# Performance work log

Measured on AMD Instinct MI355X. Metric: run time of the kernel, lower is better.

Reference implementation:

```python
import jax, jax.numpy as jnp
import numpy as np

B, V, D = 128, 1024, 512

def setup_inputs() -> dict:
    key = jax.random.key(0)
    ks = jax.random.split(key, 6)
    return {
        "features": jax.random.normal(ks[0], (B, D), dtype=jnp.float32),
        "phoneme_counts": jax.random.uniform(ks[1], (V,), minval=0.01, maxval=1.0, dtype=jnp.float32),
        "total_count": jnp.asarray(float(V), dtype=jnp.float32),
        "meg_prototypes": jax.random.normal(ks[2], (V, D), dtype=jnp.float32),
        "zipf_s": jnp.asarray(1.0, dtype=jnp.float32),
        "temperature": jnp.asarray(1.0, dtype=jnp.float32),
        "W1": jax.random.normal(ks[3], (D, 2 * D), dtype=jnp.float32) * 0.02,
        "b1": jnp.zeros((D,), dtype=jnp.float32),
        "W2": jax.random.normal(ks[4], (1, D), dtype=jnp.float32) * 0.02,
        "b2": jnp.zeros((1,), dtype=jnp.float32),
    }

def _l2norm(x, axis=-1, eps=1e-12):
    n = jnp.sqrt(jnp.sum(x * x, axis=axis, keepdims=True))
    return x / jnp.maximum(n, eps)

def reference(features, phoneme_counts, total_count, meg_prototypes,
              zipf_s, temperature, W1, b1, W2, b2):
    vocab = phoneme_counts.shape[0]
    d = features.shape[1]
    # Zipf weights: rank phonemes by frequency (descending), weight = rank^{-s}
    freqs = phoneme_counts / jnp.maximum(total_count, 1.0)
    order = jnp.argsort(-freqs)  # indices sorted by descending frequency
    ranks = jnp.zeros_like(freqs).at[order].set(
        jnp.arange(1, vocab + 1, dtype=freqs.dtype))
    zw = jnp.power(jnp.maximum(ranks, 1.0), -zipf_s)
    zipf_priors = zw / jnp.maximum(zw.sum(), 1e-8)  # [V]
    # Cosine similarity / temperature
    sim = _l2norm(features) @ _l2norm(meg_prototypes).T  # [B, V]
    sim = sim / jnp.maximum(temperature, 1e-4)
    # MLP attention: split Linear(2D,D) into feature and prototype halves,
    # avoiding the materialized [B,V,2D] concat.
    Wf, Wp = W1[:, :d], W1[:, d:]  # each [D, D]
    feat_part = features @ Wf.T          # [B, D]
    proto_part = meg_prototypes @ Wp.T   # [V, D]
    h = jax.nn.relu(feat_part[:, None, :] + proto_part[None, :, :] + b1)  # [B, V, D]
    attn = jax.nn.sigmoid(jnp.einsum('bvd,d->bv', h, W2[0]) + b2[0])      # [B, V]
    weights = zipf_priors[None, :] * (1.0 + sim) * attn
    return jax.nn.softmax(weights, axis=-1)
```

## Files before the change

### kernel.cpp

```cpp
#include <hip/hip_runtime.h>
#include <hip/hip_bf16.h>


typedef __attribute__((ext_vector_type(8))) short bhalf8;
typedef __attribute__((ext_vector_type(4))) float f32x4;

static __device__ __forceinline__ unsigned short f2bf(float x) {
    union { __hip_bfloat16 h; unsigned short u; } cv;
    cv.h = __float2bfloat16(x);
    return cv.u;
}

static __device__ __forceinline__ int4 pack_bf16_8(float4 x, float4 y) {
    union { ushort u[8]; int4 v; } r;
    r.u[0] = f2bf(x.x); r.u[1] = f2bf(x.y); r.u[2] = f2bf(x.z); r.u[3] = f2bf(x.w);
    r.u[4] = f2bf(y.x); r.u[5] = f2bf(y.y); r.u[6] = f2bf(y.z); r.u[7] = f2bf(y.w);
    return r.v;
}

__global__ __launch_bounds__(256) void gemm_prep_kernel(
    const float* __restrict__ feat, const float* __restrict__ counts,
    const float* __restrict__ proto, const float* __restrict__ zs,
    const float* __restrict__ W1, const float* __restrict__ b1,
    float* __restrict__ fpT, unsigned short* __restrict__ ppbT,
    float* __restrict__ dotraw,
    float* __restrict__ zw, float* __restrict__ invf, float* __restrict__ invp)
{
    int bx = blockIdx.x, tid = threadIdx.x;

    if (bx >= 176) {
        if (bx < 192) {
            __shared__ float cn[1024];
            ((float4*)cn)[tid] = ((const float4*)counts)[tid];
            __syncthreads();
            int il = tid >> 2, q = tid & 3;
            int i = (bx - 176) * 64 + il;
            float ci = cn[i];
            int cnt = 0;
            int j0 = q * 256;
            for (int j = j0; j < j0 + 256; ++j) {
                float cj = cn[j];
                cnt += (cj > ci) ? 1 : 0;
                cnt += (cj == ci && j < i) ? 1 : 0;
            }
            cnt += __shfl_xor(cnt, 1);
            cnt += __shfl_xor(cnt, 2);
            if (q == 0) zw[i] = powf((float)(cnt + 1), -zs[0]);
        } else {
            int nb = bx - 192;
            int w = tid >> 6, lane = tid & 63;
            int row = nb * 4 + w;
            const float* src = (row < 128) ? (feat + (size_t)row * 512)
                                           : (proto + (size_t)(row - 128) * 512);
            const float4* rp = (const float4*)src;
            float4 a = rp[lane * 2], b = rp[lane * 2 + 1];
            float ss = a.x*a.x + a.y*a.y + a.z*a.z + a.w*a.w
                     + b.x*b.x + b.y*b.y + b.z*b.z + b.w*b.w;
            for (int o = 32; o; o >>= 1) ss += __shfl_xor(ss, o);
            if (lane == 0) {
                float inv = 1.0f / fmaxf(sqrtf(ss), 1e-12f);
                if (row < 128) invf[row] = inv; else invp[row - 128] = inv;
            }
        }
        return;
    }

    const float* A; const float* Bm;
    int lda, ldb, tm, tn, mode;
    if (bx < 16) {
        A = feat; lda = 512; Bm = W1; ldb = 1024; mode = 0;
        tm = bx >> 3; tn = bx & 7;
    } else if (bx < 144) {
        int t = bx - 16;
        A = W1 + 512; lda = 1024; Bm = proto; ldb = 512; mode = 1;
        tm = t >> 4; tn = t & 15;
    } else {
        int t = bx - 144;
        A = feat; lda = 512; Bm = proto; ldb = 512; mode = 2;
        tm = t >> 4; tn = t & 15;
    }

    __shared__ unsigned short As[2][64 * 72];
    __shared__ unsigned short Bs[2][64 * 72];

    int r = tid >> 2, kq = (tid & 3) * 16;
    int wave = tid >> 6, lane = tid & 63;
    int fr = lane & 15, quad = lane >> 4;

    const float* Ag = A + (size_t)(tm * 64 + r) * lda + kq;
    const float* Bg = Bm + (size_t)(tn * 64 + r) * ldb + kq;

    float4 a0 = *(const float4*)(Ag),      a1 = *(const float4*)(Ag + 4);
    float4 a2 = *(const float4*)(Ag + 8),  a3 = *(const float4*)(Ag + 12);
    float4 g0 = *(const float4*)(Bg),      g1 = *(const float4*)(Bg + 4);
    float4 g2 = *(const float4*)(Bg + 8),  g3 = *(const float4*)(Bg + 12);

    f32x4 acc0 = {0.f, 0.f, 0.f, 0.f};
    f32x4 acc1 = acc0, acc2 = acc0, acc3 = acc0;

    for (int kc = 0; kc < 512; kc += 64) {
        int p = (kc >> 6) & 1;
        *(int4*)&As[p][r * 72 + kq]     = pack_bf16_8(a0, a1);
        *(int4*)&As[p][r * 72 + kq + 8] = pack_bf16_8(a2, a3);
        *(int4*)&Bs[p][r * 72 + kq]     = pack_bf16_8(g0, g1);
        *(int4*)&Bs[p][r * 72 + kq + 8] = pack_bf16_8(g2, g3);
        __syncthreads();
        if (kc + 64 < 512) {
            const float* An = Ag + kc + 64;
            const float* Bn = Bg + kc + 64;
            a0 = *(const float4*)(An);     a1 = *(const float4*)(An + 4);
            a2 = *(const float4*)(An + 8); a3 = *(const float4*)(An + 12);
            g0 = *(const float4*)(Bn);     g1 = *(const float4*)(Bn + 4);
            g2 = *(const float4*)(Bn + 8); g3 = *(const float4*)(Bn + 12);
        }
        #pragma unroll
        for (int s = 0; s < 2; ++s) {
            int ko = s * 32 + quad * 8;
            bhalf8 af  = *(const bhalf8*)&As[p][(wave * 16 + fr) * 72 + ko];
            bhalf8 bf0 = *(const bhalf8*)&Bs[p][(fr) * 72 + ko];
            bhalf8 bf1 = *(const bhalf8*)&Bs[p][(16 + fr) * 72 + ko];
            bhalf8 bf2 = *(const bhalf8*)&Bs[p][(32 + fr) * 72 + ko];
            bhalf8 bf3 = *(const bhalf8*)&Bs[p][(48 + fr) * 72 + ko];
            acc0 = __builtin_amdgcn_mfma_f32_16x16x32_bf16(af, bf0, acc0, 0, 0, 0);
            acc1 = __builtin_amdgcn_mfma_f32_16x16x32_bf16(af, bf1, acc1, 0, 0, 0);
            acc2 = __builtin_amdgcn_mfma_f32_16x16x32_bf16(af, bf2, acc2, 0, 0, 0);
            acc3 = __builtin_amdgcn_mfma_f32_16x16x32_bf16(af, bf3, acc3, 0, 0, 0);
        }
    }

    int m0 = tm * 64 + wave * 16 + quad * 4;
    int n0 = tn * 64 + fr;
    f32x4 accs[4] = {acc0, acc1, acc2, acc3};
    if (mode == 0) {
        for (int j = 0; j < 4; ++j)
            for (int rr = 0; rr < 4; ++rr)
                fpT[(size_t)(n0 + j * 16) * 128 + m0 + rr] = accs[j][rr];
    } else if (mode == 1) {
        float bv4[4];
        for (int rr = 0; rr < 4; ++rr) bv4[rr] = b1[m0 + rr];
        for (int j = 0; j < 4; ++j)
            for (int rr = 0; rr < 4; ++rr)
                ppbT[(size_t)(m0 + rr) * 1024 + n0 + j * 16] = f2bf(accs[j][rr] + bv4[rr]);
    } else {
        for (int j = 0; j < 4; ++j)
            for (int rr = 0; rr < 4; ++rr)
                dotraw[(size_t)(m0 + rr) * 1024 + n0 + j * 16] = accs[j][rr];
    }
}

__global__ __launch_bounds__(256) void hs_kernel(
    const float* __restrict__ fpT, const unsigned short* __restrict__ ppbT,
    const float* __restrict__ W2, float* __restrict__ hsp)
{
    int bx = blockIdx.x, tid = threadIdx.x;
    int bg = bx & 31, vh = (bx >> 5) & 1, ks = bx >> 6;
    int b0 = bg * 4, v = vh * 512 + tid * 2, k0 = ks * 32;

    float acc[4][2] = {};
    #pragma unroll 8
    for (int kk = 0; kk < 32; ++kk) {
        int k = k0 + kk;
        unsigned int u = *(const unsigned int*)(ppbT + (size_t)k * 1024 + v);
        float px = __uint_as_float(u << 16);
        float py = __uint_as_float(u & 0xffff0000u);
        float w2k = W2[k];
        float4 fa = *(const float4*)(fpT + (size_t)k * 128 + b0);
        float f[4] = {fa.x, fa.y, fa.z, fa.w};
        #pragma unroll
        for (int i = 0; i < 4; ++i) {
            acc[i][0] += fmaxf(f[i] + px, 0.f) * w2k;
            acc[i][1] += fmaxf(f[i] + py, 0.f) * w2k;
        }
    }
    float* o = hsp + ((size_t)ks * 128 + b0) * 1024 + v;
    #pragma unroll
    for (int i = 0; i < 4; ++i)
        *(float2*)(o + (size_t)i * 1024) = make_float2(acc[i][0], acc[i][1]);
}

__global__ __launch_bounds__(1024) void combine_kernel(
    const float* __restrict__ dotraw, const float* __restrict__ hsp,
    const float* __restrict__ zw,
    const float* __restrict__ invf, const float* __restrict__ invp,
    const float* __restrict__ temp, const float* __restrict__ b2,
    float* __restrict__ out)
{
    int b = blockIdx.x, tid = threadIdx.x;
    int wave = tid >> 6, lane = tid & 63;
    int v = tid;
    __shared__ float red[16];

    float it  = invf[b] / fmaxf(temp[0], 1e-4f);
    float b2v = b2[0];

    float zwv = zw[v];
    float dr  = dotraw[(size_t)b * 1024 + v];
    float ipv = invp[v];

    float h = 0.f;
    #pragma unroll
    for (int s = 0; s < 16; ++s)
        h += hsp[((size_t)s * 128 + b) * 1024 + v];

    float zs4 = zwv;
    for (int o = 32; o; o >>= 1) zs4 += __shfl_xor(zs4, o);
    if (lane == 0) red[wave] = zs4;
    __syncthreads();
    float zsum = 0.f;
    #pragma unroll
    for (int i = 0; i < 16; ++i) zsum += red[i];
    float izw = 1.0f / fmaxf(zsum, 1e-8f);
    __syncthreads();

    float sim = dr * it * ipv;
    float g = h + b2v;
    float w = (zwv * izw) * (1.0f + sim) * (1.0f / (1.0f + expf(-g)));

    float mx = w;
    for (int o = 32; o; o >>= 1) mx = fmaxf(mx, __shfl_xor(mx, o));
    if (lane == 0) red[wave] = mx;
    __syncthreads();
    mx = red[0];
    #pragma unroll
    for (int i = 1; i < 16; ++i) mx = fmaxf(mx, red[i]);
    __syncthreads();

    float e = expf(w - mx);
    float sm = e;
    for (int o = 32; o; o >>= 1) sm += __shfl_xor(sm, o);
    if (lane == 0) red[wave] = sm;
    __syncthreads();
    float tot = 0.f;
    #pragma unroll
    for (int i = 0; i < 16; ++i) tot += red[i];

    out[(size_t)b * 1024 + v] = e / tot;
}

extern "C" void kernel_launch(void* const* d_in, const int* in_sizes, int n_in,
                              void* d_out, int out_size, void* d_ws, size_t ws_size,
                              hipStream_t stream) {
    const float* feat   = (const float*)d_in[0];
    const float* counts = (const float*)d_in[1];
    const float* proto  = (const float*)d_in[3];
    const float* zs     = (const float*)d_in[4];
    const float* temp   = (const float*)d_in[5];
    const float* W1     = (const float*)d_in[6];
    const float* b1     = (const float*)d_in[7];
    const float* W2     = (const float*)d_in[8];
    const float* b2     = (const float*)d_in[9];

    char* ws = (char*)d_ws;
    float* zw     = (float*)(ws + 0);
    float* invf   = (float*)(ws + 4096);
    float* invp   = (float*)(ws + 4608);
    float* fpT    = (float*)(ws + 8704);
    float* dotraw = (float*)(ws + 270848);
    unsigned short* ppbT = (unsigned short*)(ws + 795136);
    float* hsp    = (float*)(ws + 1843712);

    gemm_prep_kernel<<<480, 256, 0, stream>>>(feat, counts, proto, zs, W1, b1,
                                              fpT, ppbT, dotraw, zw, invf, invp);
    hs_kernel<<<1024, 256, 0, stream>>>(fpT, ppbT, W2, hsp);
    combine_kernel<<<128, 1024, 0, stream>>>(dotraw, hsp, zw, invf, invp,
                                             temp, b2, (float*)d_out);
}
```

Before: 100.9 us.

## Fuse hidden-state reduction into combine kernel, drop partial-sum buffer

Moves the relu-MLP dot product into the final softmax kernel, one block per batch row with two k-halves reduced via shared memory. fp is now written row-major so each block reads its contiguous feature row. This removes a launch and the large partial-sum buffer round trip through global memory. In exchange it launches only 128 blocks and loses the 4-row register reuse of prototype loads, lengthening the serial per-thread loop.

```diff
diff --git a/kernel.cpp b/kernel.cpp
--- a/kernel.cpp
+++ b/kernel.cpp
@@ -22,7 +22,7 @@
     const float* __restrict__ feat, const float* __restrict__ counts,
     const float* __restrict__ proto, const float* __restrict__ zs,
     const float* __restrict__ W1, const float* __restrict__ b1,
-    float* __restrict__ fpT, unsigned short* __restrict__ ppbT,
+    float* __restrict__ fp, unsigned short* __restrict__ ppbT,
     float* __restrict__ dotraw,
     float* __restrict__ zw, float* __restrict__ invf, float* __restrict__ invp)
 {
@@ -134,7 +134,7 @@
     if (mode == 0) {
         for (int j = 0; j < 4; ++j)
             for (int rr = 0; rr < 4; ++rr)
-                fpT[(size_t)(n0 + j * 16) * 128 + m0 + rr] = accs[j][rr];
+                fp[(size_t)(m0 + rr) * 512 + n0 + j * 16] = accs[j][rr];
     } else if (mode == 1) {
         float bv4[4];
         for (int rr = 0; rr < 4; ++rr) bv4[rr] = b1[m0 + rr];
@@ -148,59 +148,47 @@
     }
 }
 
-__global__ __launch_bounds__(256) void hs_kernel(
-    const float* __restrict__ fpT, const unsigned short* __restrict__ ppbT,
-    const float* __restrict__ W2, float* __restrict__ hsp)
-{
-    int bx = blockIdx.x, tid = threadIdx.x;
-    int bg = bx & 31, vh = (bx >> 5) & 1, ks = bx >> 6;
-    int b0 = bg * 4, v = vh * 512 + tid * 2, k0 = ks * 32;
-
-    float acc[4][2] = {};
-    #pragma unroll 8
-    for (int kk = 0; kk < 32; ++kk) {
-        int k = k0 + kk;
-        unsigned int u = *(const unsigned int*)(ppbT + (size_t)k * 1024 + v);
-        float px = __uint_as_float(u << 16);
-        float py = __uint_as_float(u & 0xffff0000u);
-        float w2k = W2[k];
-        float4 fa = *(const float4*)(fpT + (size_t)k * 128 + b0);
-        float f[4] = {fa.x, fa.y, fa.z, fa.w};
-        #pragma unroll
-        for (int i = 0; i < 4; ++i) {
-            acc[i][0] += fmaxf(f[i] + px, 0.f) * w2k;
-            acc[i][1] += fmaxf(f[i] + py, 0.f) * w2k;
-        }
-    }
-    float* o = hsp + ((size_t)ks * 128 + b0) * 1024 + v;
-    #pragma unroll
-    for (int i = 0; i < 4; ++i)
-        *(float2*)(o + (size_t)i * 1024) = make_float2(acc[i][0], acc[i][1]);
-}
-
-__global__ __launch_bounds__(1024) void combine_kernel(
-    const float* __restrict__ dotraw, const float* __restrict__ hsp,
-    const float* __restrict__ zw,
+__global__ __launch_bounds__(1024) void fused_kernel(
+    const float* __restrict__ fp, const unsigned short* __restrict__ ppbT,
+    const float* __restrict__ W2,
+    const float* __restrict__ dotraw, const float* __restrict__ zw,
     const float* __restrict__ invf, const float* __restrict__ invp,
     const float* __restrict__ temp, const float* __restrict__ b2,
     float* __restrict__ out)
 {
     int b = blockIdx.x, tid = threadIdx.x;
+    int vp = tid & 511, kh = tid >> 9;
+
+    const float* fpb = fp + (size_t)b * 512 + kh * 256;
+    const float* w2b = W2 + kh * 256;
+    const unsigned short* pb = ppbT + (size_t)(kh * 256) * 1024 + vp * 2;
+
+    float a0[2] = {0.f, 0.f}, a1[2] = {0.f, 0.f};
+    #pragma unroll 8
+    for (int kk = 0; kk < 256; ++kk) {
+        unsigned int u = *(const unsigned int*)(pb + (size_t)kk * 1024);
+        float px = __uint_as_float(u << 16);
+        float py = __uint_as_float(u & 0xffff0000u);
+        float w2k = w2b[kk];
+        float fk  = fpb[kk];
+        a0[kk & 1] += fmaxf(fk + px, 0.f) * w2k;
+        a1[kk & 1] += fmaxf(fk + py, 0.f) * w2k;
+    }
+
+    __shared__ float hred[2][1024];
+    *(float2*)&hred[kh][vp * 2] = make_float2(a0[0] + a0[1], a1[0] + a1[1]);
+    __syncthreads();
+
     int wave = tid >> 6, lane = tid & 63;
     int v = tid;
     __shared__ float red[16];
 
+    float h   = hred[0][v] + hred[1][v];
     float it  = invf[b] / fmaxf(temp[0], 1e-4f);
     float b2v = b2[0];
-
     float zwv = zw[v];
     float dr  = dotraw[(size_t)b * 1024 + v];
     float ipv = invp[v];
-
-    float h = 0.f;
-    #pragma unroll
-    for (int s = 0; s < 16; ++s)
-        h += hsp[((size_t)s * 128 + b) * 1024 + v];
 
     float zs4 = zwv;
     for (int o = 32; o; o >>= 1) zs4 += __shfl_xor(zs4, o);
@@ -254,14 +242,12 @@
     float* zw     = (float*)(ws + 0);
     float* invf   = (float*)(ws + 4096);
     float* invp   = (float*)(ws + 4608);
-    float* fpT    = (float*)(ws + 8704);
+    float* fp     = (float*)(ws + 8704);
     float* dotraw = (float*)(ws + 270848);
     unsigned short* ppbT = (unsigned short*)(ws + 795136);
-    float* hsp    = (float*)(ws + 1843712);
 
     gemm_prep_kernel<<<480, 256, 0, stream>>>(feat, counts, proto, zs, W1, b1,
-                                              fpT, ppbT, dotraw, zw, invf, invp);
-    hs_kernel<<<1024, 256, 0, stream>>>(fpT, ppbT, W2, hsp);
-    combine_kernel<<<128, 1024, 0, stream>>>(dotraw, hsp, zw, invf, invp,
-                                             temp, b2, (float*)d_out);
-}
+                                              fp, ppbT, dotraw, zw, invf, invp);
+    fused_kernel<<<128, 1024, 0, stream>>>(fp, ppbT, W2, dotraw, zw, invf, invp,
+                                           temp, b2, (float*)d_out);
+}
```

After: 111.3 us. 1.1x slower.
